# Kernel tuning notes

Measured on AMD Instinct MI355X. Metric: run time of the kernel, lower is better.

## Reference

```python
import jax, jax.numpy as jnp
import numpy as np

B, NPG, D = 512, 200, 256  # graphs, nodes-per-graph, d_model
N = B * NPG
STEP = 4


def setup_inputs() -> dict:
    key = jax.random.key(0)
    ks = jax.random.split(key, 7)
    def xav(k, shape):
        fan_in, fan_out = shape[1], shape[0]
        std = float(np.sqrt(2.0 / (fan_in + fan_out)))
        return jax.random.normal(k, shape, jnp.float32) * std
    return {
        "node": jax.random.normal(ks[0], (N, D), jnp.float32),
        "node_num": jnp.full((B,), NPG, dtype=jnp.int32),
        "W_ih": xav(ks[1], (4 * D, 2 * D)),  # lstm weight_ih_l0
        "W_hh": xav(ks[2], (4 * D, D)),      # lstm weight_hh_l0
        "b_ih": jnp.zeros((4 * D,), jnp.float32),
        "b_hh": jnp.zeros((4 * D,), jnp.float32),
        "Wo": xav(ks[3], (D, 2 * D)),        # W_o.weight
        "bo": jnp.zeros((D,), jnp.float32),  # W_o.bias
    }


def reference(node, node_num, W_ih, W_hh, b_ih, b_hh, Wo, bo):
    n_total, d = node.shape
    bsz = node_num.shape[0]
    batch_idx = jnp.repeat(jnp.arange(bsz), node_num, total_repeat_length=n_total)
    h = jnp.zeros((bsz, d), node.dtype)
    c = jnp.zeros((bsz, d), node.dtype)
    q_star = jnp.zeros((bsz, 2 * d), node.dtype)
    for _ in range(STEP):
        # single-step LSTM (torch gate order: i, f, g, o)
        gates = q_star @ W_ih.T + h @ W_hh.T + b_ih + b_hh
        i, f, g, o = jnp.split(gates, 4, axis=-1)
        c = jax.nn.sigmoid(f) * c + jax.nn.sigmoid(i) * jnp.tanh(g)
        h = jax.nn.sigmoid(o) * jnp.tanh(c)
        q = h  # [B, d]
        # segmented softmax attention over nodes
        e = jnp.sum(node * q[batch_idx], axis=-1)  # [N]
        emax = jax.ops.segment_max(e, batch_idx, num_segments=bsz)
        e = jnp.exp(e - emax[batch_idx])
        denom = jax.ops.segment_sum(e, batch_idx, num_segments=bsz)
        a = e / (denom[batch_idx] + 1e-6)
        r = jax.ops.segment_sum(a[:, None] * node, batch_idx, num_segments=bsz)
        q_star = jnp.concatenate([q, r], axis=-1)
    return q_star @ Wo.T + bo
```

## Files before the change

kernel.cpp:

```cpp
#include <hip/hip_runtime.h>
#include <math.h>

#define DCH 256
#define BSZ 512
#define NPG 200
#define G4  1024
#define K2  512
#define KSD 8

__device__ __forceinline__ float sigf(float x) { return 1.0f / (1.0f + __expf(-x)); }

__device__ __forceinline__ unsigned pack2bf(float a, float b) {
    unsigned ua = __float_as_uint(a), ub = __float_as_uint(b);
    ua = (ua + 0x7FFFu + ((ua >> 16) & 1u)) >> 16;
    ub = (ub + 0x7FFFu + ((ub >> 16) & 1u)) & 0xFFFF0000u;
    return ua | ub;
}
__device__ __forceinline__ float lo_bf(unsigned u) { return __uint_as_float(u << 16); }
__device__ __forceinline__ float hi_bf(unsigned u) { return __uint_as_float(u & 0xFFFF0000u); }

__global__ __launch_bounds__(256) void gemm_gates_kernel(
    const float* __restrict__ A, const float* __restrict__ Bm,
    const float* __restrict__ Whh, float* __restrict__ Cpart, int Kper)
{
    __shared__ __align__(16) float As[32][132];
    __shared__ __align__(16) float Bs[32][68];
    const int tid = threadIdx.x;
    const int bm = blockIdx.y * 128, bn = blockIdx.x * 64;
    const int kbase = blockIdx.z * Kper;
    const int tx = tid & 15, ty = tid >> 4;
    float acc[8][4] = {};

    for (int k0 = 0; k0 < Kper; k0 += 32) {
        const int kg = kbase + k0;
        const bool addhh = (kg < DCH);
        #pragma unroll
        for (int i = 0; i < 4; ++i) {
            const int id = tid + i * 256;
            const int r = id >> 3, cc = id & 7;
            const float4 v = *(const float4*)(A + (size_t)(bm + r) * K2 + kg + 4 * cc);
            As[4*cc+0][r] = v.x; As[4*cc+1][r] = v.y; As[4*cc+2][r] = v.z; As[4*cc+3][r] = v.w;
        }
        #pragma unroll
        for (int i = 0; i < 2; ++i) {
            const int id = tid + i * 256;
            const int r = id >> 3, cc = id & 7;
            float4 u = *(const float4*)(Bm + (size_t)(bn + r) * K2 + kg + 4 * cc);
            if (addhh) {
                const float4 h4 = *(const float4*)(Whh + (size_t)(bn + r) * DCH + kg + 4 * cc);
                u.x += h4.x; u.y += h4.y; u.z += h4.z; u.w += h4.w;
            }
            Bs[4*cc+0][r] = u.x; Bs[4*cc+1][r] = u.y; Bs[4*cc+2][r] = u.z; Bs[4*cc+3][r] = u.w;
        }
        __syncthreads();
        #pragma unroll
        for (int kk = 0; kk < 32; ++kk) {
            const float4 alo = *(const float4*)(&As[kk][8 * ty]);
            const float4 ahi = *(const float4*)(&As[kk][8 * ty + 4]);
            const float4 b4  = *(const float4*)(&Bs[kk][4 * tx]);
            acc[0][0] += alo.x * b4.x; acc[0][1] += alo.x * b4.y; acc[0][2] += alo.x * b4.z; acc[0][3] += alo.x * b4.w;
            acc[1][0] += alo.y * b4.x; acc[1][1] += alo.y * b4.y; acc[1][2] += alo.y * b4.z; acc[1][3] += alo.y * b4.w;
            acc[2][0] += alo.z * b4.x; acc[2][1] += alo.z * b4.y; acc[2][2] += alo.z * b4.z; acc[2][3] += alo.z * b4.w;
            acc[3][0] += alo.w * b4.x; acc[3][1] += alo.w * b4.y; acc[3][2] += alo.w * b4.z; acc[3][3] += alo.w * b4.w;
            acc[4][0] += ahi.x * b4.x; acc[4][1] += ahi.x * b4.y; acc[4][2] += ahi.x * b4.z; acc[4][3] += ahi.x * b4.w;
            acc[5][0] += ahi.y * b4.x; acc[5][1] += ahi.y * b4.y; acc[5][2] += ahi.y * b4.z; acc[5][3] += ahi.y * b4.w;
            acc[6][0] += ahi.z * b4.x; acc[6][1] += ahi.z * b4.y; acc[6][2] += ahi.z * b4.z; acc[6][3] += ahi.z * b4.w;
            acc[7][0] += ahi.w * b4.x; acc[7][1] += ahi.w * b4.y; acc[7][2] += ahi.w * b4.z; acc[7][3] += ahi.w * b4.w;
        }
        __syncthreads();
    }

    float* Cp = Cpart + (size_t)blockIdx.z * BSZ * G4;
    #pragma unroll
    for (int i = 0; i < 8; ++i) {
        float4 o;
        o.x = acc[i][0]; o.y = acc[i][1]; o.z = acc[i][2]; o.w = acc[i][3];
        *(float4*)(Cp + (size_t)(bm + 8 * ty + i) * G4 + bn + 4 * tx) = o;
    }
}

template<int FIRST, int LAST>
__global__ __launch_bounds__(256) void lstm_attn_kernel(
    const float* __restrict__ gpart,
    const float* __restrict__ b_ih, const float* __restrict__ b_hh,
    const float* __restrict__ node, uint4* __restrict__ nbf,
    const int* __restrict__ node_num,
    float* __restrict__ cbuf, float* __restrict__ hr,
    const float* __restrict__ Wo, const float* __restrict__ bo,
    float* __restrict__ outp)
{
    __shared__ __align__(16) float smem[4640];
    float* qs = smem;
    float (*red_r)[DCH] = (float (*)[DCH])(smem + 512);
    float* red_m = smem + 4608;
    float* red_s = smem + 4624;

    const int b = blockIdx.x;
    const int t = threadIdx.x;

    float gv[4];
    #pragma unroll
    for (int q = 0; q < 4; ++q) {
        const int idx = q * DCH + t;
        float v = b_ih[idx] + b_hh[idx];
        if (!FIRST) {
            #pragma unroll
            for (int z = 0; z < KSD; ++z)
                v += gpart[(size_t)z * BSZ * G4 + (size_t)b * G4 + idx];
        }
        gv[q] = v;
    }
    const float c_old = FIRST ? 0.0f : cbuf[b * DCH + t];
    const float cn = sigf(gv[1]) * c_old + sigf(gv[0]) * tanhf(gv[2]);
    const float hn = sigf(gv[3]) * tanhf(cn);
    if (!LAST) {
        cbuf[b * DCH + t] = cn;
        hr[(size_t)b * K2 + t] = hn;
    }
    qs[t] = hn;
    __syncthreads();

    const int w = t >> 6, l = t & 63;
    const int p = l & 15;
    const int g = w * 4 + (l >> 4);
    const int cnt = node_num[b];
    const float* nb = node + (size_t)b * NPG * DCH;
    uint4* nbf_b = nbf + (size_t)b * NPG * 32;

    float4 qv[4];
    #pragma unroll
    for (int j = 0; j < 2; ++j) {
        qv[j*2+0] = *(const float4*)(qs + j * 128 + p * 8);
        qv[j*2+1] = *(const float4*)(qs + j * 128 + p * 8 + 4);
    }

    auto ld_f32 = [&](int n, float4* x) {
        if (n < cnt) {
            #pragma unroll
            for (int j = 0; j < 2; ++j) {
                x[j*2+0] = *(const float4*)(nb + (size_t)n * DCH + j * 128 + p * 8);
                x[j*2+1] = *(const float4*)(nb + (size_t)n * DCH + j * 128 + p * 8 + 4);
            }
        } else {
            x[0] = x[1] = x[2] = x[3] = make_float4(0.f, 0.f, 0.f, 0.f);
        }
    };
    auto ld_bf = [&](int n, float4* x) {
        if (n < cnt) {
            #pragma unroll
            for (int j = 0; j < 2; ++j) {
                const uint4 u = nbf_b[(size_t)n * 32 + j * 16 + p];
                x[j*2+0] = make_float4(lo_bf(u.x), hi_bf(u.x), lo_bf(u.y), hi_bf(u.y));
                x[j*2+1] = make_float4(lo_bf(u.z), hi_bf(u.z), lo_bf(u.w), hi_bf(u.w));
            }
        } else {
            x[0] = x[1] = x[2] = x[3] = make_float4(0.f, 0.f, 0.f, 0.f);
        }
    };
    auto st_bf = [&](int n, const float4* x) {
        if (n < cnt) {
            #pragma unroll
            for (int j = 0; j < 2; ++j) {
                uint4 u;
                u.x = pack2bf(x[j*2+0].x, x[j*2+0].y);
                u.y = pack2bf(x[j*2+0].z, x[j*2+0].w);
                u.z = pack2bf(x[j*2+1].x, x[j*2+1].y);
                u.w = pack2bf(x[j*2+1].z, x[j*2+1].w);
                nbf_b[(size_t)n * 32 + j * 16 + p] = u;
            }
        }
    };

    float m = -INFINITY, s = 0.0f;
    float4 racc[4] = {};
    const int nit = (cnt + 31) >> 5;

    float4 x0[4], x1[4];
    if (FIRST) { ld_f32(2 * g, x0); ld_f32(2 * g + 1, x1); }
    else       { ld_bf (2 * g, x0); ld_bf (2 * g + 1, x1); }

    for (int it = 0; it < nit; ++it) {
        const int n0 = it * 32 + 2 * g;
        const int np = n0 + 32;
        float4 y0[4], y1[4];
        if (FIRST) { ld_f32(np, y0); ld_f32(np + 1, y1); }
        else       { ld_bf (np, y0); ld_bf (np + 1, y1); }
        if (FIRST) { st_bf(n0, x0); st_bf(n0 + 1, x1); }

        float e0 = 0.f, e1 = 0.f;
        #pragma unroll
        for (int j = 0; j < 4; ++j) {
            e0 += x0[j].x * qv[j].x + x0[j].y * qv[j].y + x0[j].z * qv[j].z + x0[j].w * qv[j].w;
            e1 += x1[j].x * qv[j].x + x1[j].y * qv[j].y + x1[j].z * qv[j].z + x1[j].w * qv[j].w;
        }
        #pragma unroll
        for (int off = 1; off < 16; off <<= 1) {
            e0 += __shfl_xor(e0, off);
            e1 += __shfl_xor(e1, off);
        }
        if (n0     >= cnt) e0 = -INFINITY;
        if (n0 + 1 >= cnt) e1 = -INFINITY;
        const float mn = fmaxf(m, fmaxf(e0, e1));
        if (mn > -INFINITY) {
            const float sc = __expf(m - mn);
            const float w0 = __expf(e0 - mn);
            const float w1 = __expf(e1 - mn);
            s = s * sc + w0 + w1;
            #pragma unroll
            for (int j = 0; j < 4; ++j) {
                racc[j].x = racc[j].x * sc + w0 * x0[j].x + w1 * x1[j].x;
                racc[j].y = racc[j].y * sc + w0 * x0[j].y + w1 * x1[j].y;
                racc[j].z = racc[j].z * sc + w0 * x0[j].z + w1 * x1[j].z;
                racc[j].w = racc[j].w * sc + w0 * x0[j].w + w1 * x1[j].w;
            }
            m = mn;
        }
        #pragma unroll
        for (int j = 0; j < 4; ++j) { x0[j] = y0[j]; x1[j] = y1[j]; }
    }

    #pragma unroll
    for (int j = 0; j < 2; ++j) {
        *(float4*)(&red_r[g][j * 128 + p * 8])     = racc[j*2+0];
        *(float4*)(&red_r[g][j * 128 + p * 8 + 4]) = racc[j*2+1];
    }
    if (p == 0) { red_m[g] = m; red_s[g] = s; }
    __syncthreads();

    float M = -INFINITY;
    #pragma unroll
    for (int g2 = 0; g2 < 16; ++g2) M = fmaxf(M, red_m[g2]);
    float stot = 0.0f, rtot = 0.0f;
    #pragma unroll
    for (int g2 = 0; g2 < 16; ++g2) {
        const float sc = __expf(red_m[g2] - M);
        stot += sc * red_s[g2];
        rtot += sc * red_r[g2][t];
    }
    rtot = rtot / (stot + 1e-6f);

    if (!LAST) {
        hr[(size_t)b * K2 + DCH + t] = rtot;
        return;
    }

    qs[256 + t] = rtot;
    __syncthreads();

    float4 qv2[8];
    #pragma unroll
    for (int j = 0; j < 4; ++j) {
        qv2[j*2+0] = *(const float4*)(qs + j * 128 + p * 8);
        qv2[j*2+1] = *(const float4*)(qs + j * 128 + p * 8 + 4);
    }
    float* out_sm = smem + 512;

    #pragma unroll 2
    for (int v = 0; v < 8; ++v) {
        const int o0 = (2 * v) * 16 + g;
        const int o1 = o0 + 16;
        float e0 = 0.f, e1 = 0.f;
        #pragma unroll
        for (int j = 0; j < 4; ++j) {
            const float4 wa0 = *(const float4*)(Wo + (size_t)o0 * K2 + j * 128 + p * 8);
            const float4 wa1 = *(const float4*)(Wo + (size_t)o0 * K2 + j * 128 + p * 8 + 4);
            const float4 wb0 = *(const float4*)(Wo + (size_t)o1 * K2 + j * 128 + p * 8);
            const float4 wb1 = *(const float4*)(Wo + (size_t)o1 * K2 + j * 128 + p * 8 + 4);
            e0 += wa0.x * qv2[j*2].x + wa0.y * qv2[j*2].y + wa0.z * qv2[j*2].z + wa0.w * qv2[j*2].w;
            e0 += wa1.x * qv2[j*2+1].x + wa1.y * qv2[j*2+1].y + wa1.z * qv2[j*2+1].z + wa1.w * qv2[j*2+1].w;
            e1 += wb0.x * qv2[j*2].x + wb0.y * qv2[j*2].y + wb0.z * qv2[j*2].z + wb0.w * qv2[j*2].w;
            e1 += wb1.x * qv2[j*2+1].x + wb1.y * qv2[j*2+1].y + wb1.z * qv2[j*2+1].z + wb1.w * qv2[j*2+1].w;
        }
        #pragma unroll
        for (int off = 1; off < 16; off <<= 1) {
            e0 += __shfl_xor(e0, off);
            e1 += __shfl_xor(e1, off);
        }
        if (p == 0) {
            out_sm[o0] = e0 + bo[o0];
            out_sm[o1] = e1 + bo[o1];
        }
    }
    __syncthreads();
    outp[(size_t)b * DCH + t] = out_sm[t];
}

extern "C" void kernel_launch(void* const* d_in, const int* in_sizes, int n_in,
                              void* d_out, int out_size, void* d_ws, size_t ws_size,
                              hipStream_t stream)
{
    const float* node     = (const float*)d_in[0];
    const int*   node_num = (const int*)  d_in[1];
    const float* W_ih     = (const float*)d_in[2];
    const float* W_hh     = (const float*)d_in[3];
    const float* b_ih     = (const float*)d_in[4];
    const float* b_hh     = (const float*)d_in[5];
    const float* Wo       = (const float*)d_in[6];
    const float* bo       = (const float*)d_in[7];
    float* out = (float*)d_out;

    float* ws    = (float*)d_ws;
    float* cbuf  = ws;
    float* hr    = cbuf + BSZ * DCH;
    float* gpart = hr + BSZ * K2;
    uint4* nbf   = (uint4*)(gpart + (size_t)KSD * BSZ * G4);

    lstm_attn_kernel<1, 0><<<BSZ, 256, 0, stream>>>(
        gpart, b_ih, b_hh, node, nbf, node_num, cbuf, hr, Wo, bo, out);

    for (int s = 1; s < 4; ++s) {
        gemm_gates_kernel<<<dim3(G4 / 64, BSZ / 128, KSD), 256, 0, stream>>>(
            hr, W_ih, W_hh, gpart, K2 / KSD);
        if (s < 3) {
            lstm_attn_kernel<0, 0><<<BSZ, 256, 0, stream>>>(
                gpart, b_ih, b_hh, node, nbf, node_num, cbuf, hr, Wo, bo, out);
        } else {
            lstm_attn_kernel<0, 1><<<BSZ, 256, 0, stream>>>(
                gpart, b_ih, b_hh, node, nbf, node_num, cbuf, hr, Wo, bo, out);
        }
    }
}
```

Measured before the change: 120.8 us.

## Switch gate GEMM to bf16 MFMA with prepacked fused weights

A prep kernel adds W_hh into W_ih and converts the result, along with Wo, to bf16 once per call. The scalar-FMA gate GEMM is replaced with an MFMA 16x16x32 bf16 kernel that reads bf16 activations written directly by the attention kernel, and the split-K factor drops from 8 to 4. This removes the per-tile W_hh add and shrinks gate-weight and output-projection traffic. The cost is an extra launch and reduced precision from bf16 operands. The MFMA kernel loads operands straight from global memory without LDS staging and writes output with scalar stores.

```diff
diff --git a/kernel.cpp b/kernel.cpp
--- a/kernel.cpp
+++ b/kernel.cpp
@@ -6,7 +6,10 @@
 #define NPG 200
 #define G4  1024
 #define K2  512
-#define KSD 8
+#define KSD 4
+
+typedef __attribute__((ext_vector_type(8))) short short8v;
+typedef __attribute__((ext_vector_type(4))) float f32x4;
 
 __device__ __forceinline__ float sigf(float x) { return 1.0f / (1.0f + __expf(-x)); }
 
@@ -19,64 +22,86 @@
 __device__ __forceinline__ float lo_bf(unsigned u) { return __uint_as_float(u << 16); }
 __device__ __forceinline__ float hi_bf(unsigned u) { return __uint_as_float(u & 0xFFFF0000u); }
 
-__global__ __launch_bounds__(256) void gemm_gates_kernel(
-    const float* __restrict__ A, const float* __restrict__ Bm,
-    const float* __restrict__ Whh, float* __restrict__ Cpart, int Kper)
+__global__ __launch_bounds__(256) void prep_kernel(
+    const float* __restrict__ W_ih, const float* __restrict__ W_hh,
+    const float* __restrict__ Wo,
+    uint4* __restrict__ wcat, uint4* __restrict__ wobf)
 {
-    __shared__ __align__(16) float As[32][132];
-    __shared__ __align__(16) float Bs[32][68];
-    const int tid = threadIdx.x;
-    const int bm = blockIdx.y * 128, bn = blockIdx.x * 64;
+    int idx = blockIdx.x * 256 + threadIdx.x;
+    if (idx < 65536) {
+        const int n = idx >> 6, k = (idx & 63) * 8;
+        float v[8];
+        *(float4*)(v)     = *(const float4*)(W_ih + (size_t)n * K2 + k);
+        *(float4*)(v + 4) = *(const float4*)(W_ih + (size_t)n * K2 + k + 4);
+        if (k < DCH) {
+            float h[8];
+            *(float4*)(h)     = *(const float4*)(W_hh + (size_t)n * DCH + k);
+            *(float4*)(h + 4) = *(const float4*)(W_hh + (size_t)n * DCH + k + 4);
+            #pragma unroll
+            for (int i = 0; i < 8; ++i) v[i] += h[i];
+        }
+        uint4 u;
+        u.x = pack2bf(v[0], v[1]); u.y = pack2bf(v[2], v[3]);
+        u.z = pack2bf(v[4], v[5]); u.w = pack2bf(v[6], v[7]);
+        wcat[idx] = u;
+    } else {
+        idx -= 65536;
+        const int n = idx >> 6, k = (idx & 63) * 8;
+        float v[8];
+        *(float4*)(v)     = *(const float4*)(Wo + (size_t)n * K2 + k);
+        *(float4*)(v + 4) = *(const float4*)(Wo + (size_t)n * K2 + k + 4);
+        uint4 u;
+        u.x = pack2bf(v[0], v[1]); u.y = pack2bf(v[2], v[3]);
+        u.z = pack2bf(v[4], v[5]); u.w = pack2bf(v[6], v[7]);
+        wobf[idx] = u;
+    }
+}
+
+__global__ __launch_bounds__(256) void gemm_gates_mfma(
+    const unsigned short* __restrict__ hrbf,
+    const unsigned short* __restrict__ wcat,
+    float* __restrict__ gpart, int Kper)
+{
+    const int wid  = threadIdx.x >> 6;
+    const int lane = threadIdx.x & 63;
+    const int bm = blockIdx.y * 64;
+    const int bn = blockIdx.x * 128 + wid * 32;
     const int kbase = blockIdx.z * Kper;
-    const int tx = tid & 15, ty = tid >> 4;
-    float acc[8][4] = {};
+    const int rsel = lane & 15, kgrp = lane >> 4;
+
+    f32x4 acc00 = {}, acc01 = {}, acc10 = {}, acc11 = {},
+          acc20 = {}, acc21 = {}, acc30 = {}, acc31 = {};
 
     for (int k0 = 0; k0 < Kper; k0 += 32) {
-        const int kg = kbase + k0;
-        const bool addhh = (kg < DCH);
-        #pragma unroll
-        for (int i = 0; i < 4; ++i) {
-            const int id = tid + i * 256;
-            const int r = id >> 3, cc = id & 7;
-            const float4 v = *(const float4*)(A + (size_t)(bm + r) * K2 + kg + 4 * cc);
-            As[4*cc+0][r] = v.x; As[4*cc+1][r] = v.y; As[4*cc+2][r] = v.z; As[4*cc+3][r] = v.w;
-        }
-        #pragma unroll
-        for (int i = 0; i < 2; ++i) {
-            const int id = tid + i * 256;
-            const int r = id >> 3, cc = id & 7;
-            float4 u = *(const float4*)(Bm + (size_t)(bn + r) * K2 + kg + 4 * cc);
-            if (addhh) {
-                const float4 h4 = *(const float4*)(Whh + (size_t)(bn + r) * DCH + kg + 4 * cc);
-                u.x += h4.x; u.y += h4.y; u.z += h4.z; u.w += h4.w;
-            }
-            Bs[4*cc+0][r] = u.x; Bs[4*cc+1][r] = u.y; Bs[4*cc+2][r] = u.z; Bs[4*cc+3][r] = u.w;
-        }
-        __syncthreads();
-        #pragma unroll
-        for (int kk = 0; kk < 32; ++kk) {
-            const float4 alo = *(const float4*)(&As[kk][8 * ty]);
-            const float4 ahi = *(const float4*)(&As[kk][8 * ty + 4]);
-            const float4 b4  = *(const float4*)(&Bs[kk][4 * tx]);
-            acc[0][0] += alo.x * b4.x; acc[0][1] += alo.x * b4.y; acc[0][2] += alo.x * b4.z; acc[0][3] += alo.x * b4.w;
-            acc[1][0] += alo.y * b4.x; acc[1][1] += alo.y * b4.y; acc[1][2] += alo.y * b4.z; acc[1][3] += alo.y * b4.w;
-            acc[2][0] += alo.z * b4.x; acc[2][1] += alo.z * b4.y; acc[2][2] += alo.z * b4.z; acc[2][3] += alo.z * b4.w;
-            acc[3][0] += alo.w * b4.x; acc[3][1] += alo.w * b4.y; acc[3][2] += alo.w * b4.z; acc[3][3] += alo.w * b4.w;
-            acc[4][0] += ahi.x * b4.x; acc[4][1] += ahi.x * b4.y; acc[4][2] += ahi.x * b4.z; acc[4][3] += ahi.x * b4.w;
-            acc[5][0] += ahi.y * b4.x; acc[5][1] += ahi.y * b4.y; acc[5][2] += ahi.y * b4.z; acc[5][3] += ahi.y * b4.w;
-            acc[6][0] += ahi.z * b4.x; acc[6][1] += ahi.z * b4.y; acc[6][2] += ahi.z * b4.z; acc[6][3] += ahi.z * b4.w;
-            acc[7][0] += ahi.w * b4.x; acc[7][1] += ahi.w * b4.y; acc[7][2] += ahi.w * b4.z; acc[7][3] += ahi.w * b4.w;
-        }
-        __syncthreads();
-    }
-
-    float* Cp = Cpart + (size_t)blockIdx.z * BSZ * G4;
-    #pragma unroll
-    for (int i = 0; i < 8; ++i) {
-        float4 o;
-        o.x = acc[i][0]; o.y = acc[i][1]; o.z = acc[i][2]; o.w = acc[i][3];
-        *(float4*)(Cp + (size_t)(bm + 8 * ty + i) * G4 + bn + 4 * tx) = o;
-    }
+        const int kk = kbase + k0 + kgrp * 8;
+        short8v a0 = *(const short8v*)(hrbf + (size_t)(bm +  0 + rsel) * K2 + kk);
+        short8v a1 = *(const short8v*)(hrbf + (size_t)(bm + 16 + rsel) * K2 + kk);
+        short8v a2 = *(const short8v*)(hrbf + (size_t)(bm + 32 + rsel) * K2 + kk);
+        short8v a3 = *(const short8v*)(hrbf + (size_t)(bm + 48 + rsel) * K2 + kk);
+        short8v b0 = *(const short8v*)(wcat + (size_t)(bn +  0 + rsel) * K2 + kk);
+        short8v b1 = *(const short8v*)(wcat + (size_t)(bn + 16 + rsel) * K2 + kk);
+        acc00 = __builtin_amdgcn_mfma_f32_16x16x32_bf16(a0, b0, acc00, 0, 0, 0);
+        acc01 = __builtin_amdgcn_mfma_f32_16x16x32_bf16(a0, b1, acc01, 0, 0, 0);
+        acc10 = __builtin_amdgcn_mfma_f32_16x16x32_bf16(a1, b0, acc10, 0, 0, 0);
+        acc11 = __builtin_amdgcn_mfma_f32_16x16x32_bf16(a1, b1, acc11, 0, 0, 0);
+        acc20 = __builtin_amdgcn_mfma_f32_16x16x32_bf16(a2, b0, acc20, 0, 0, 0);
+        acc21 = __builtin_amdgcn_mfma_f32_16x16x32_bf16(a2, b1, acc21, 0, 0, 0);
+        acc30 = __builtin_amdgcn_mfma_f32_16x16x32_bf16(a3, b0, acc30, 0, 0, 0);
+        acc31 = __builtin_amdgcn_mfma_f32_16x16x32_bf16(a3, b1, acc31, 0, 0, 0);
+    }
+
+    float* Cp = gpart + (size_t)blockIdx.z * BSZ * G4;
+    const int crow = kgrp * 4, ccol = rsel;
+    const f32x4* accs[4][2] = { {&acc00, &acc01}, {&acc10, &acc11},
+                                {&acc20, &acc21}, {&acc30, &acc31} };
+    #pragma unroll
+    for (int mi = 0; mi < 4; ++mi)
+        #pragma unroll
+        for (int ni = 0; ni < 2; ++ni)
+            #pragma unroll
+            for (int r = 0; r < 4; ++r)
+                Cp[(size_t)(bm + mi * 16 + crow + r) * G4 + bn + ni * 16 + ccol] =
+                    (*accs[mi][ni])[r];
 }
 
 template<int FIRST, int LAST>
@@ -85,8 +110,8 @@
     const float* __restrict__ b_ih, const float* __restrict__ b_hh,
     const float* __restrict__ node, uint4* __restrict__ nbf,
     const int* __restrict__ node_num,
-    float* __restrict__ cbuf, float* __restrict__ hr,
-    const float* __restrict__ Wo, const float* __restrict__ bo,
+    float* __restrict__ cbuf, unsigned* __restrict__ hrbf,
+    const uint4* __restrict__ wobf, const float* __restrict__ bo,
     float* __restrict__ outp)
 {
     __shared__ __align__(16) float smem[4640];
@@ -113,10 +138,7 @@
     const float c_old = FIRST ? 0.0f : cbuf[b * DCH + t];
     const float cn = sigf(gv[1]) * c_old + sigf(gv[0]) * tanhf(gv[2]);
     const float hn = sigf(gv[3]) * tanhf(cn);
-    if (!LAST) {
-        cbuf[b * DCH + t] = cn;
-        hr[(size_t)b * K2 + t] = hn;
-    }
+    if (!LAST) cbuf[b * DCH + t] = cn;
     qs[t] = hn;
     __syncthreads();
 
@@ -239,13 +261,13 @@
     }
     rtot = rtot / (stot + 1e-6f);
 
-    if (!LAST) {
-        hr[(size_t)b * K2 + DCH + t] = rtot;
-        return;
-    }
-
     qs[256 + t] = rtot;
     __syncthreads();
+
+    if (!LAST) {
+        hrbf[b * 256 + t] = pack2bf(qs[2 * t], qs[2 * t + 1]);
+        return;
+    }
 
     float4 qv2[8];
     #pragma unroll
@@ -262,14 +284,16 @@
         float e0 = 0.f, e1 = 0.f;
         #pragma unroll
         for (int j = 0; j < 4; ++j) {
-            const float4 wa0 = *(const float4*)(Wo + (size_t)o0 * K2 + j * 128 + p * 8);
-            const float4 wa1 = *(const float4*)(Wo + (size_t)o0 * K2 + j * 128 + p * 8 + 4);
-            const float4 wb0 = *(const float4*)(Wo + (size_t)o1 * K2 + j * 128 + p * 8);
-            const float4 wb1 = *(const float4*)(Wo + (size_t)o1 * K2 + j * 128 + p * 8 + 4);
-            e0 += wa0.x * qv2[j*2].x + wa0.y * qv2[j*2].y + wa0.z * qv2[j*2].z + wa0.w * qv2[j*2].w;
-            e0 += wa1.x * qv2[j*2+1].x + wa1.y * qv2[j*2+1].y + wa1.z * qv2[j*2+1].z + wa1.w * qv2[j*2+1].w;
-            e1 += wb0.x * qv2[j*2].x + wb0.y * qv2[j*2].y + wb0.z * qv2[j*2].z + wb0.w * qv2[j*2].w;
-            e1 += wb1.x * qv2[j*2+1].x + wb1.y * qv2[j*2+1].y + wb1.z * qv2[j*2+1].z + wb1.w * qv2[j*2+1].w;
+            const uint4 ua = wobf[(size_t)o0 * 64 + j * 16 + p];
+            const uint4 ub = wobf[(size_t)o1 * 64 + j * 16 + p];
+            e0 += lo_bf(ua.x) * qv2[j*2].x + hi_bf(ua.x) * qv2[j*2].y
+                + lo_bf(ua.y) * qv2[j*2].z + hi_bf(ua.y) * qv2[j*2].w
+                + lo_bf(ua.z) * qv2[j*2+1].x + hi_bf(ua.z) * qv2[j*2+1].y
+                + lo_bf(ua.w) * qv2[j*2+1].z + hi_bf(ua.w) * qv2[j*2+1].w;
+            e1 += lo_bf(ub.x) * qv2[j*2].x + hi_bf(ub.x) * qv2[j*2].y
+                + lo_bf(ub.y) * qv2[j*2].z + hi_bf(ub.y) * qv2[j*2].w
+                + lo_bf(ub.z) * qv2[j*2+1].x + hi_bf(ub.z) * qv2[j*2+1].y
+                + lo_bf(ub.w) * qv2[j*2+1].z + hi_bf(ub.w) * qv2[j*2+1].w;
         }
         #pragma unroll
         for (int off = 1; off < 16; off <<= 1) {
@@ -299,24 +323,28 @@
     const float* bo       = (const float*)d_in[7];
     float* out = (float*)d_out;
 
-    float* ws    = (float*)d_ws;
-    float* cbuf  = ws;
-    float* hr    = cbuf + BSZ * DCH;
-    float* gpart = hr + BSZ * K2;
-    uint4* nbf   = (uint4*)(gpart + (size_t)KSD * BSZ * G4);
+    float* ws      = (float*)d_ws;
+    float* cbuf    = ws;
+    unsigned* hrbf = (unsigned*)(cbuf + BSZ * DCH);
+    float* gpart   = (float*)(hrbf + BSZ * 256);
+    uint4* wcat    = (uint4*)(gpart + (size_t)KSD * BSZ * G4);
+    uint4* wobf    = wcat + 1024 * 64;
+    uint4* nbf     = wobf + 256 * 64;
+
+    prep_kernel<<<320, 256, 0, stream>>>(W_ih, W_hh, Wo, wcat, wobf);
 
     lstm_attn_kernel<1, 0><<<BSZ, 256, 0, stream>>>(
-        gpart, b_ih, b_hh, node, nbf, node_num, cbuf, hr, Wo, bo, out);
+        gpart, b_ih, b_hh, node, nbf, node_num, cbuf, hrbf, wobf, bo, out);
 
     for (int s = 1; s < 4; ++s) {
-        gemm_gates_kernel<<<dim3(G4 / 64, BSZ / 128, KSD), 256, 0, stream>>>(
-            hr, W_ih, W_hh, gpart, K2 / KSD);
+        gemm_gates_mfma<<<dim3(8, 8, KSD), 256, 0, stream>>>(
+            (const unsigned short*)hrbf, (const unsigned short*)wcat, gpart, K2 / KSD);
         if (s < 3) {
             lstm_attn_kernel<0, 0><<<BSZ, 256, 0, stream>>>(
-                gpart, b_ih, b_hh, node, nbf, node_num, cbuf, hr, Wo, bo, out);
+                gpart, b_ih, b_hh, node, nbf, node_num, cbuf, hrbf, wobf, bo, out);
         } else {
             lstm_attn_kernel<0, 1><<<BSZ, 256, 0, stream>>>(
-                gpart, b_ih, b_hh, node, nbf, node_num, cbuf, hr, Wo, bo, out);
-        }
-    }
-}
+                gpart, b_ih, b_hh, node, nbf, node_num, cbuf, hrbf, wobf, bo, out);
+        }
+    }
+}
```

Result: faster. 102.7 us (-15.0%).
